# Optimization experiments

Hardware: AMD Instinct MI355X
Metric: run time of the kernel (lower is better)

The kernel has to match this reference:

```python
import jax, jax.numpy as jnp
import numpy as np

N_NODES = 10000
N_EDGES = 320000
IN_FEATS = 500
CONV_DIMS = [500, 256, 256]
FC_DIMS = [256, 128, 40]
BN_EPS = 1e-5


def setup_inputs() -> dict:
    key = jax.random.key(0)
    ks = jax.random.split(key, 16)
    inp = {
        "x": jax.random.normal(ks[0], (N_NODES, IN_FEATS), dtype=jnp.float32),
        "edge_index": jax.random.randint(ks[1], (2, N_EDGES), 0, N_NODES, dtype=jnp.int64),
    }
    # conv layer params: Linear W [in,out], b [out]; BatchNorm gamma/beta [out]
    ki = 2
    for li in range(len(CONV_DIMS) - 1):
        d_in, d_out = CONV_DIMS[li], CONV_DIMS[li + 1]
        s = 1.0 / np.sqrt(d_in)
        inp[f"conv_W{li}"] = jax.random.uniform(ks[ki], (d_in, d_out), jnp.float32, -s, s); ki += 1
        inp[f"conv_b{li}"] = jax.random.uniform(ks[ki], (d_out,), jnp.float32, -s, s); ki += 1
        inp[f"bn_g{li}"] = jnp.ones((d_out,), jnp.float32)
        inp[f"bn_b{li}"] = jnp.zeros((d_out,), jnp.float32)
    for li in range(len(FC_DIMS) - 1):
        d_in, d_out = FC_DIMS[li], FC_DIMS[li + 1]
        s = 1.0 / np.sqrt(d_in)
        inp[f"fc_W{li}"] = jax.random.uniform(ks[ki], (d_in, d_out), jnp.float32, -s, s); ki += 1
        inp[f"fc_b{li}"] = jax.random.uniform(ks[ki], (d_out,), jnp.float32, -s, s); ki += 1
    return inp


def _degree(edge_index, n, dtype):
    # Faithful to: A = eye(N); A[i,j] = 1 per edge (set semantics dedupes repeats).
    A = jnp.eye(n, dtype=dtype).at[edge_index[0], edge_index[1]].set(1.0)
    return A.sum(axis=1)  # deg_i = rowsum of A


def _batchnorm(h, g, b):
    # training-mode BatchNorm1d: batch stats, biased variance
    mean = h.mean(axis=0)
    var = h.var(axis=0)
    return (h - mean) * jax.lax.rsqrt(var + BN_EPS) * g + b


def reference(x, edge_index, conv_W0, conv_b0, bn_g0, bn_b0,
              conv_W1, conv_b1, bn_g1, bn_b1,
              fc_W0, fc_b0, fc_W1, fc_b1):
    n = x.shape[0]
    deg = _degree(edge_index, n, x.dtype)
    # D = sqrt(diag(deg)) is a diagonal matrix, so elementwise D*A*D = diag(deg);
    # mm(D*A*D, x) == deg[:, None] * x (exactly the original math).
    h = x
    for W, b, g, beta in ((conv_W0, conv_b0, bn_g0, bn_b0),
                          (conv_W1, conv_b1, bn_g1, bn_b1)):
        h = (deg[:, None] * h) @ W + b
        h = jax.nn.relu(h)
        h = _batchnorm(h, g, beta)
        # dropout: identity at inference
    for W, b in ((fc_W0, fc_b0), (fc_W1, fc_b1)):
        h = jax.nn.relu(h @ W + b)  # original appends ReLU after every fc, incl. last
    return h
```

## Files before the change

### kernel.cpp

```cpp
#include <hip/hip_runtime.h>

#define NN 10000
#define NE 320000
#define ROW_WORDS 320
#define MP 10112
#define BN_EPS 1e-5f

typedef __attribute__((ext_vector_type(8))) short short8;
typedef __attribute__((ext_vector_type(4))) float f32x4;
typedef unsigned short u16;

__device__ __forceinline__ void split1(float v, u16& h, u16& l) {
    unsigned int u = __float_as_uint(v);
    h = (u16)(u >> 16);
    float hf = __uint_as_float(u & 0xFFFF0000u);
    l = (u16)(__float_as_uint(v - hf) >> 16);
}

__device__ __forceinline__ void gll16(const void* g, void* l) {
    __builtin_amdgcn_global_load_lds(
        (const __attribute__((address_space(1))) unsigned int*)g,
        (__attribute__((address_space(3))) unsigned int*)l, 16, 0, 0);
}

__device__ void splitW_dev(const float* __restrict__ W, int K, int N, int Kp, int Np,
                           u16* __restrict__ Wt, int bx, int by, char* smem) {
    float (*tile)[65] = (float(*)[65])smem;
    int t = threadIdx.x;
    int bk = bx * 64, bn = by * 64;
    #pragma unroll
    for (int p = 0; p < 4; ++p) {
        int kk = (t >> 4) + p * 16;
        int nc = (t & 15) * 4;
        int k = bk + kk;
        float4 v = {0.f, 0.f, 0.f, 0.f};
        if (k < K && bn + nc + 3 < N)
            v = *(const float4*)&W[(size_t)k * N + bn + nc];
        tile[kk][nc] = v.x; tile[kk][nc + 1] = v.y;
        tile[kk][nc + 2] = v.z; tile[kk][nc + 3] = v.w;
    }
    __syncthreads();
    int nn = t >> 2;
    int kk0 = (t & 3) * 16;
    u16 hs[16], ls[16];
    #pragma unroll
    for (int j = 0; j < 16; ++j) split1(tile[kk0 + j][nn], hs[j], ls[j]);
    size_t ob = (size_t)(bn + nn) * Kp + bk + kk0;
    size_t lo = (size_t)Np * Kp;
    *(short8*)&Wt[ob] = *(short8*)hs;
    *(short8*)&Wt[ob + 8] = *(short8*)&hs[8];
    *(short8*)&Wt[lo + ob] = *(short8*)ls;
    *(short8*)&Wt[lo + ob + 8] = *(short8*)&ls[8];
}

__device__ void xsplit_dev(const float* __restrict__ x, u16* __restrict__ xs, int gblk) {
    int t = threadIdx.x;
    int r0 = gblk * 16 + (t >> 4);
    int l = t & 15;
    u16* xlo = xs + (size_t)MP * 512;
    #pragma unroll
    for (int j = 0; j < 8; ++j) {
        int k = (l + j * 16) * 4;
        float vals[4] = {0.f, 0.f, 0.f, 0.f};
        if (r0 < NN && k < 500) {
            float4 v = *(const float4*)&x[(size_t)r0 * 500 + k];
            vals[0] = v.x; vals[1] = v.y; vals[2] = v.z; vals[3] = v.w;
        }
        ushort4 hs, ls;
        split1(vals[0], hs.x, ls.x); split1(vals[1], hs.y, ls.y);
        split1(vals[2], hs.z, ls.z); split1(vals[3], hs.w, ls.w);
        *(ushort4*)&xs[(size_t)r0 * 512 + k] = hs;
        *(ushort4*)&xlo[(size_t)r0 * 512 + k] = ls;
    }
}

__global__ __launch_bounds__(256)
void scatter_prep(const int* __restrict__ ei, unsigned int* __restrict__ bitmap,
                  const float* __restrict__ x,
                  const float* __restrict__ W0, const float* __restrict__ fW1,
                  u16* __restrict__ xs, u16* __restrict__ W0t, u16* __restrict__ fW1t) {
    __shared__ char smem[16704];
    int b = blockIdx.x;
    if (b < 1290) {
        int e = b * 256 + threadIdx.x;
        if (e < NE + NN) {
            int i, j;
            if (e < NE) { i = ei[e]; j = ei[NE + e]; }
            else        { i = e - NE; j = i; }
            atomicOr(&bitmap[i * ROW_WORDS + (j >> 5)], 1u << (j & 31));
        }
    } else if (b < 1922) {
        xsplit_dev(x, xs, b - 1290);
    } else if (b < 1954) {
        int idx = b - 1922;
        splitW_dev(W0, 500, 256, 512, 256, W0t, idx & 7, idx >> 3, smem);
    } else {
        splitW_dev(fW1, 128, 40, 128, 64, fW1t, b - 1954, 0, smem);
    }
}

__global__ __launch_bounds__(256, 4)
void conv0_gemm(const u16* __restrict__ Ahi, const u16* __restrict__ Alo,
                const u16* __restrict__ Bhi, const u16* __restrict__ Blo,
                const unsigned int* __restrict__ bitmap, const float* __restrict__ bias,
                float* __restrict__ deg, float* __restrict__ stats,
                u16* __restrict__ Ohi, u16* __restrict__ Olo) {
    __shared__ char smem[32768];
    __shared__ float sdeg[64];
    const int Kp = 512, M = NN, No = 256;
    const int b = blockIdx.x;
    const int xcd = b & 7, g = b >> 3;
    const int bx = g & 3, by = (g >> 2) * 8 + xcd;
    if (by >= 158) return;
    const int t = threadIdx.x;
    const int lane = t & 63;
    const int w = t >> 6;
    const int q = lane >> 4;
    const int l16 = lane & 15;
    const int m7 = l16 & 7;
    const int row0 = by * 64;
    const int col0 = bx * 64;

    const u16* bases[4] = {Ahi, Alo, Bhi, Blo};
    const u16* srcs[8];
    unsigned dstoff[8];
    #pragma unroll
    for (int i = 0; i < 8; ++i) {
        int gi = w + i * 4;
        int reg = i >> 1;
        int j = gi & 7;
        int rb = (reg < 2) ? row0 : col0;
        int r = j * 8 + (lane >> 3);
        int c = (lane & 7) ^ (r & 7);
        srcs[i] = bases[reg] + (size_t)(rb + r) * Kp + c * 8;
        dstoff[i] = reg * 8192 + j * 1024;
    }

    f32x4 acc[4];
    #pragma unroll
    for (int s = 0; s < 4; ++s) acc[s] = (f32x4){0.f, 0.f, 0.f, 0.f};

    #pragma unroll
    for (int i = 0; i < 8; ++i) { gll16(srcs[i], smem + dstoff[i]); srcs[i] += 64; }

    {
        int rr = t >> 2, wl = t & 3;
        int grow = row0 + rr;
        int cnt = 0;
        if (grow < NN)
            for (int wd = wl; wd < ROW_WORDS; wd += 4)
                cnt += __popc(bitmap[(size_t)grow * ROW_WORDS + wd]);
        cnt += __shfl_down(cnt, 1, 4);
        cnt += __shfl_down(cnt, 2, 4);
        if (wl == 0) {
            sdeg[rr] = (float)cnt;
            if (bx == 0 && grow < NN) deg[grow] = (float)cnt;
        }
    }

    for (int k0 = 0; k0 < Kp; k0 += 64) {
        __syncthreads();
        short8 ah[2], al[2], bh[2][4], bl[2][4];
        #pragma unroll
        for (int kc = 0; kc < 2; ++kc) {
            int aoff = (w * 16 + l16) * 128 + (((kc * 4 + q) ^ m7) * 16);
            ah[kc] = *(const short8*)(smem + aoff);
            al[kc] = *(const short8*)(smem + 8192 + aoff);
            #pragma unroll
            for (int s = 0; s < 4; ++s) {
                int boff = (s * 16 + l16) * 128 + (((kc * 4 + q) ^ m7) * 16);
                bh[kc][s] = *(const short8*)(smem + 16384 + boff);
                bl[kc][s] = *(const short8*)(smem + 24576 + boff);
            }
        }
        __syncthreads();
        if (k0 + 64 < Kp) {
            #pragma unroll
            for (int i = 0; i < 8; ++i) { gll16(srcs[i], smem + dstoff[i]); srcs[i] += 64; }
        }
        #pragma unroll
        for (int kc = 0; kc < 2; ++kc)
            #pragma unroll
            for (int s = 0; s < 4; ++s) {
                acc[s] = __builtin_amdgcn_mfma_f32_16x16x32_bf16(al[kc], bh[kc][s], acc[s], 0, 0, 0);
                acc[s] = __builtin_amdgcn_mfma_f32_16x16x32_bf16(ah[kc], bl[kc][s], acc[s], 0, 0, 0);
                acc[s] = __builtin_amdgcn_mfma_f32_16x16x32_bf16(ah[kc], bh[kc][s], acc[s], 0, 0, 0);
            }
    }

    int growb = row0 + w * 16 + q * 4;
    float dgv[4];
    #pragma unroll
    for (int r = 0; r < 4; ++r) {
        int grow = growb + r;
        dgv[r] = (grow < M) ? sdeg[grow - row0] : 0.f;
    }
    #pragma unroll
    for (int s = 0; s < 4; ++s) {
        int gc = col0 + s * 16 + l16;
        float bia = bias[gc];
        float s_sum = 0.f, ss_sum = 0.f;
        #pragma unroll
        for (int r = 0; r < 4; ++r) {
            int grow = growb + r;
            bool real = grow < M;
            float v = fmaxf(fmaf(dgv[r], acc[s][r], bia), 0.f);
            if (!real) v = 0.f;
            s_sum += v; ss_sum += v * v;
            float vo = v * dgv[r];
            u16 h, l; split1(vo, h, l);
            Ohi[(size_t)grow * No + gc] = h;
            Olo[(size_t)grow * No + gc] = l;
        }
        s_sum  += __shfl_xor(s_sum, 16);  s_sum  += __shfl_xor(s_sum, 32);
        ss_sum += __shfl_xor(ss_sum, 16); ss_sum += __shfl_xor(ss_sum, 32);
        if (lane < 16) {
            atomicAdd(&stats[gc], s_sum);
            atomicAdd(&stats[256 + gc], ss_sum);
        }
    }
}

__global__ __launch_bounds__(256, 4)
void conv1_fold(const u16* __restrict__ Ahi, const u16* __restrict__ Alo,
                const float* __restrict__ W1, const float* __restrict__ stats0,
                const float* __restrict__ g0, const float* __restrict__ bb0,
                const float* __restrict__ b1, const float* __restrict__ deg,
                float* __restrict__ stats1, u16* __restrict__ Ohi, u16* __restrict__ Olo) {
    __shared__ char smem[32768];
    __shared__ float scl[256], sh[256], cred[256], cvec[64];
    const int Kp = 256, M = NN, No = 256;
    const int b = blockIdx.x;
    const int xcd = b & 7, g = b >> 3;
    const int bx = g & 3, by = (g >> 2) * 8 + xcd;
    if (by >= 158) return;
    const int t = threadIdx.x;
    const int lane = t & 63;
    const int w = t >> 6;
    const int q = lane >> 4;
    const int l16 = lane & 15;
    const int m7 = l16 & 7;
    const int row0 = by * 64;
    const int col0 = bx * 64;

    const u16* srcs[4];
    unsigned dstoff[4];
    #pragma unroll
    for (int i = 0; i < 4; ++i) {
        int gi = w + i * 4;
        int plane = gi >> 3, j = gi & 7;
        int r = j * 8 + (lane >> 3);
        int c = (lane & 7) ^ (r & 7);
        srcs[i] = (plane ? Alo : Ahi) + (size_t)(row0 + r) * Kp + c * 8;
        dstoff[i] = plane * 8192 + j * 1024;
    }
    #pragma unroll
    for (int i = 0; i < 4; ++i) { gll16(srcs[i], smem + dstoff[i]); srcs[i] += 64; }

    {
        float mean = stats0[t] * (1.f / NN);
        float var = stats0[256 + t] * (1.f / NN) - mean * mean;
        float s = g0[t] * rsqrtf(var + BN_EPS);
        scl[t] = s;
        sh[t] = bb0[t] - mean * s;
    }
    __syncthreads();
    {
        float s = 0.f;
        int n = col0 + (t & 63);
        #pragma unroll 8
        for (int k = (t >> 6); k < 256; k += 4)
            s += sh[k] * W1[(size_t)k * 256 + n];
        cred[t] = s;
        __syncthreads();
        if (t < 64) cvec[t] = cred[t] + cred[t + 64] + cred[t + 128] + cred[t + 192];
    }
    const int bn = t & 63;
    const int kb = (t >> 6) * 16;
    const int ch0 = (t >> 6) * 2;
    float vals[16];
    {
        const float* wp = W1 + (size_t)kb * 256 + col0 + bn;
        #pragma unroll
        for (int i = 0; i < 16; ++i) vals[i] = wp[(size_t)i * 256] * scl[kb + i];
    }

    f32x4 acc[4];
    #pragma unroll
    for (int s = 0; s < 4; ++s) acc[s] = (f32x4){0.f, 0.f, 0.f, 0.f};

    for (int k0 = 0; k0 < Kp; k0 += 64) {
        {
            u16 hs[16], ls[16];
            #pragma unroll
            for (int i = 0; i < 16; ++i) split1(vals[i], hs[i], ls[i]);
            unsigned o0 = bn * 128 + ((ch0 ^ (bn & 7)) * 16);
            unsigned o1 = bn * 128 + (((ch0 + 1) ^ (bn & 7)) * 16);
            *(short8*)(smem + 16384 + o0) = *(short8*)&hs[0];
            *(short8*)(smem + 16384 + o1) = *(short8*)&hs[8];
            *(short8*)(smem + 24576 + o0) = *(short8*)&ls[0];
            *(short8*)(smem + 24576 + o1) = *(short8*)&ls[8];
        }
        __syncthreads();
        short8 ah[2], al[2], bh[2][4], bl[2][4];
        #pragma unroll
        for (int kc = 0; kc < 2; ++kc) {
            int aoff = (w * 16 + l16) * 128 + (((kc * 4 + q) ^ m7) * 16);
            ah[kc] = *(const short8*)(smem + aoff);
            al[kc] = *(const short8*)(smem + 8192 + aoff);
            #pragma unroll
            for (int s = 0; s < 4; ++s) {
                int boff = (s * 16 + l16) * 128 + (((kc * 4 + q) ^ m7) * 16);
                bh[kc][s] = *(const short8*)(smem + 16384 + boff);
                bl[kc][s] = *(const short8*)(smem + 24576 + boff);
            }
        }
        __syncthreads();
        if (k0 + 64 < Kp) {
            #pragma unroll
            for (int i = 0; i < 4; ++i) { gll16(srcs[i], smem + dstoff[i]); srcs[i] += 64; }
            const float* wp = W1 + (size_t)(k0 + 64 + kb) * 256 + col0 + bn;
            #pragma unroll
            for (int i = 0; i < 16; ++i) vals[i] = wp[(size_t)i * 256] * scl[k0 + 64 + kb + i];
        }
        #pragma unroll
        for (int kc = 0; kc < 2; ++kc)
            #pragma unroll
            for (int s = 0; s < 4; ++s) {
                acc[s] = __builtin_amdgcn_mfma_f32_16x16x32_bf16(al[kc], bh[kc][s], acc[s], 0, 0, 0);
                acc[s] = __builtin_amdgcn_mfma_f32_16x16x32_bf16(ah[kc], bl[kc][s], acc[s], 0, 0, 0);
                acc[s] = __builtin_amdgcn_mfma_f32_16x16x32_bf16(ah[kc], bh[kc][s], acc[s], 0, 0, 0);
            }
    }

    int growb = row0 + w * 16 + q * 4;
    float dgv[4];
    #pragma unroll
    for (int r = 0; r < 4; ++r) dgv[r] = (growb + r < M) ? deg[growb + r] : 0.f;
    #pragma unroll
    for (int s = 0; s < 4; ++s) {
        int gc = col0 + s * 16 + l16;
        float bia = b1[gc];
        float cv = cvec[s * 16 + l16];
        float s_sum = 0.f, ss_sum = 0.f;
        #pragma unroll
        for (int r = 0; r < 4; ++r) {
            int grow = growb + r;
            bool real = grow < M;
            float v = fmaxf(fmaf(dgv[r], cv, acc[s][r] + bia), 0.f);
            if (!real) v = 0.f;
            s_sum += v; ss_sum += v * v;
            u16 h, l; split1(v, h, l);
            Ohi[(size_t)grow * No + gc] = h;
            Olo[(size_t)grow * No + gc] = l;
        }
        s_sum  += __shfl_xor(s_sum, 16);  s_sum  += __shfl_xor(s_sum, 32);
        ss_sum += __shfl_xor(ss_sum, 16); ss_sum += __shfl_xor(ss_sum, 32);
        if (lane < 16) {
            atomicAdd(&stats1[gc], s_sum);
            atomicAdd(&stats1[256 + gc], ss_sum);
        }
    }
}

__global__ __launch_bounds__(256, 4)
void fc0_fold(const u16* __restrict__ Ahi, const u16* __restrict__ Alo,
              const float* __restrict__ fW0, const float* __restrict__ stats1,
              const float* __restrict__ g1, const float* __restrict__ bb1,
              const float* __restrict__ fb0,
              u16* __restrict__ Ohi, u16* __restrict__ Olo) {
    __shared__ char smem[32768];
    __shared__ float scl[256], sh[256], cred[256], biasf[64];
    const int Kp = 256, M = NN, No = 128;
    const int b = blockIdx.x;
    const int xcd = b & 7, g = b >> 3;
    const int bx = g & 1, by = (g >> 1) * 8 + xcd;
    if (by >= 158) return;
    const int t = threadIdx.x;
    const int lane = t & 63;
    const int w = t >> 6;
    const int q = lane >> 4;
    const int l16 = lane & 15;
    const int m7 = l16 & 7;
    const int row0 = by * 64;
    const int col0 = bx * 64;

    const u16* srcs[4];
    unsigned dstoff[4];
    #pragma unroll
    for (int i = 0; i < 4; ++i) {
        int gi = w + i * 4;
        int plane = gi >> 3, j = gi & 7;
        int r = j * 8 + (lane >> 3);
        int c = (lane & 7) ^ (r & 7);
        srcs[i] = (plane ? Alo : Ahi) + (size_t)(row0 + r) * Kp + c * 8;
        dstoff[i] = plane * 8192 + j * 1024;
    }
    #pragma unroll
    for (int i = 0; i < 4; ++i) { gll16(srcs[i], smem + dstoff[i]); srcs[i] += 64; }

    {
        float mean = stats1[t] * (1.f / NN);
        float var = stats1[256 + t] * (1.f / NN) - mean * mean;
        float s = g1[t] * rsqrtf(var + BN_EPS);
        scl[t] = s;
        sh[t] = bb1[t] - mean * s;
    }
    __syncthreads();
    {
        float s = 0.f;
        int n = col0 + (t & 63);
        #pragma unroll 8
        for (int k = (t >> 6); k < 256; k += 4)
            s += sh[k] * fW0[(size_t)k * 128 + n];
        cred[t] = s;
        __syncthreads();
        if (t < 64)
            biasf[t] = fb0[col0 + t] + cred[t] + cred[t + 64] + cred[t + 128] + cred[t + 192];
    }
    const int bn = t & 63;
    const int kb = (t >> 6) * 16;
    const int ch0 = (t >> 6) * 2;
    float vals[16];
    {
        const float* wp = fW0 + (size_t)kb * 128 + col0 + bn;
        #pragma unroll
        for (int i = 0; i < 16; ++i) vals[i] = wp[(size_t)i * 128] * scl[kb + i];
    }

    f32x4 acc[4];
    #pragma unroll
    for (int s = 0; s < 4; ++s) acc[s] = (f32x4){0.f, 0.f, 0.f, 0.f};

    for (int k0 = 0; k0 < Kp; k0 += 64) {
        {
            u16 hs[16], ls[16];
            #pragma unroll
            for (int i = 0; i < 16; ++i) split1(vals[i], hs[i], ls[i]);
            unsigned o0 = bn * 128 + ((ch0 ^ (bn & 7)) * 16);
            unsigned o1 = bn * 128 + (((ch0 + 1) ^ (bn & 7)) * 16);
            *(short8*)(smem + 16384 + o0) = *(short8*)&hs[0];
            *(short8*)(smem + 16384 + o1) = *(short8*)&hs[8];
            *(short8*)(smem + 24576 + o0) = *(short8*)&ls[0];
            *(short8*)(smem + 24576 + o1) = *(short8*)&ls[8];
        }
        __syncthreads();
        short8 ah[2], al[2], bh[2][4], bl[2][4];
        #pragma unroll
        for (int kc = 0; kc < 2; ++kc) {
            int aoff = (w * 16 + l16) * 128 + (((kc * 4 + q) ^ m7) * 16);
            ah[kc] = *(const short8*)(smem + aoff);
            al[kc] = *(const short8*)(smem + 8192 + aoff);
            #pragma unroll
            for (int s = 0; s < 4; ++s) {
                int boff = (s * 16 + l16) * 128 + (((kc * 4 + q) ^ m7) * 16);
                bh[kc][s] = *(const short8*)(smem + 16384 + boff);
                bl[kc][s] = *(const short8*)(smem + 24576 + boff);
            }
        }
        __syncthreads();
        if (k0 + 64 < Kp) {
            #pragma unroll
            for (int i = 0; i < 4; ++i) { gll16(srcs[i], smem + dstoff[i]); srcs[i] += 64; }
            const float* wp = fW0 + (size_t)(k0 + 64 + kb) * 128 + col0 + bn;
            #pragma unroll
            for (int i = 0; i < 16; ++i) vals[i] = wp[(size_t)i * 128] * scl[k0 + 64 + kb + i];
        }
        #pragma unroll
        for (int kc = 0; kc < 2; ++kc)
            #pragma unroll
            for (int s = 0; s < 4; ++s) {
                acc[s] = __builtin_amdgcn_mfma_f32_16x16x32_bf16(al[kc], bh[kc][s], acc[s], 0, 0, 0);
                acc[s] = __builtin_amdgcn_mfma_f32_16x16x32_bf16(ah[kc], bl[kc][s], acc[s], 0, 0, 0);
                acc[s] = __builtin_amdgcn_mfma_f32_16x16x32_bf16(ah[kc], bh[kc][s], acc[s], 0, 0, 0);
            }
    }

    int growb = row0 + w * 16 + q * 4;
    #pragma unroll
    for (int s = 0; s < 4; ++s) {
        int gc = col0 + s * 16 + l16;
        float bia = biasf[s * 16 + l16];
        #pragma unroll
        for (int r = 0; r < 4; ++r) {
            int grow = growb + r;
            float v = fmaxf(acc[s][r] + bia, 0.f);
            if (grow >= M) v = 0.f;
            u16 h, l; split1(v, h, l);
            Ohi[(size_t)grow * No + gc] = h;
            Olo[(size_t)grow * No + gc] = l;
        }
    }
}

__global__ __launch_bounds__(256, 3)
void fc1_gemm(const u16* __restrict__ Ahi, const u16* __restrict__ Alo,
              const u16* __restrict__ Bhi, const u16* __restrict__ Blo,
              const float* __restrict__ bias, float* __restrict__ out) {
    __shared__ char smem[32768];
    const int Kp = 128, M = NN, N = 40, No = 40;
    const int t = threadIdx.x;
    const int lane = t & 63;
    const int w = t >> 6;
    const int q = lane >> 4;
    const int l16 = lane & 15;
    const int m7 = l16 & 7;
    const int row0 = blockIdx.x * 64;
    const int col0 = 0;

    const u16* bases[4] = {Ahi, Alo, Bhi, Blo};
    const u16* srcs[8];
    unsigned dstoff[8];
    #pragma unroll
    for (int i = 0; i < 8; ++i) {
        int gi = w + i * 4;
        int reg = i >> 1;
        int j = gi & 7;
        int rb = (reg < 2) ? row0 : col0;
        int r = j * 8 + (lane >> 3);
        int c = (lane & 7) ^ (r & 7);
        srcs[i] = bases[reg] + (size_t)(rb + r) * Kp + c * 8;
        dstoff[i] = reg * 8192 + j * 1024;
    }

    f32x4 acc[4];
    #pragma unroll
    for (int s = 0; s < 4; ++s) acc[s] = (f32x4){0.f, 0.f, 0.f, 0.f};

    #pragma unroll
    for (int i = 0; i < 8; ++i) { gll16(srcs[i], smem + dstoff[i]); srcs[i] += 64; }

    for (int k0 = 0; k0 < Kp; k0 += 64) {
        __syncthreads();
        short8 ah[2], al[2], bh[2][4], bl[2][4];
        #pragma unroll
        for (int kc = 0; kc < 2; ++kc) {
            int aoff = (w * 16 + l16) * 128 + (((kc * 4 + q) ^ m7) * 16);
            ah[kc] = *(const short8*)(smem + aoff);
            al[kc] = *(const short8*)(smem + 8192 + aoff);
            #pragma unroll
            for (int s = 0; s < 4; ++s) {
                int boff = (s * 16 + l16) * 128 + (((kc * 4 + q) ^ m7) * 16);
                bh[kc][s] = *(const short8*)(smem + 16384 + boff);
                bl[kc][s] = *(const short8*)(smem + 24576 + boff);
            }
        }
        __syncthreads();
        if (k0 + 64 < Kp) {
            #pragma unroll
            for (int i = 0; i < 8; ++i) { gll16(srcs[i], smem + dstoff[i]); srcs[i] += 64; }
        }
        #pragma unroll
        for (int kc = 0; kc < 2; ++kc)
            #pragma unroll
            for (int s = 0; s < 4; ++s) {
                acc[s] = __builtin_amdgcn_mfma_f32_16x16x32_bf16(al[kc], bh[kc][s], acc[s], 0, 0, 0);
                acc[s] = __builtin_amdgcn_mfma_f32_16x16x32_bf16(ah[kc], bl[kc][s], acc[s], 0, 0, 0);
                acc[s] = __builtin_amdgcn_mfma_f32_16x16x32_bf16(ah[kc], bh[kc][s], acc[s], 0, 0, 0);
            }
    }

    int growb = row0 + w * 16 + q * 4;
    #pragma unroll
    for (int s = 0; s < 4; ++s) {
        int gc = col0 + s * 16 + l16;
        if (gc >= N) continue;
        float bia = bias[gc];
        #pragma unroll
        for (int r = 0; r < 4; ++r) {
            int grow = growb + r;
            if (grow < M)
                out[(size_t)grow * No + gc] = fmaxf(acc[s][r] + bia, 0.f);
        }
    }
}


extern "C" void kernel_launch(void* const* d_in, const int* in_sizes, int n_in,
                              void* d_out, int out_size, void* d_ws, size_t ws_size,
                              hipStream_t stream) {
    const float* x   = (const float*)d_in[0];
    const int*   ei  = (const int*)d_in[1];
    const float* W0  = (const float*)d_in[2];
    const float* b0  = (const float*)d_in[3];
    const float* g0  = (const float*)d_in[4];
    const float* bb0 = (const float*)d_in[5];
    const float* W1  = (const float*)d_in[6];
    const float* b1  = (const float*)d_in[7];
    const float* g1  = (const float*)d_in[8];
    const float* bb1 = (const float*)d_in[9];
    const float* fW0 = (const float*)d_in[10];
    const float* fb0 = (const float*)d_in[11];
    const float* fW1 = (const float*)d_in[12];
    const float* fb1 = (const float*)d_in[13];
    float* out = (float*)d_out;

    char* ws = (char*)d_ws;
    auto carve = [&](size_t bytes) { char* q = ws; ws += (bytes + 255) & ~(size_t)255; return q; };

    const size_t BITMAP_BYTES = (size_t)NN * ROW_WORDS * 4;
    char* region0 = carve(BITMAP_BYTES + 4096);
    unsigned int* bitmap = (unsigned int*)region0;
    float* stats = (float*)(region0 + BITMAP_BYTES);

    float* deg  = (float*)carve(MP * 4);
    u16* xs     = (u16*)carve((size_t)2 * MP * 512 * 2);
    u16* W0t    = (u16*)carve((size_t)2 * 256 * 512 * 2);
    u16* fW1t   = (u16*)carve((size_t)2 * 64 * 128 * 2);
    u16* H1     = (u16*)carve((size_t)2 * MP * 256 * 2);
    u16* H2     = (u16*)carve((size_t)2 * MP * 256 * 2);
    u16* H3     = (u16*)carve((size_t)2 * MP * 128 * 2);

    dim3 blk(256);

    hipMemsetAsync(region0, 0, BITMAP_BYTES + 4096, stream);
    scatter_prep<<<1956, blk, 0, stream>>>(ei, bitmap, x, W0, fW1, xs, W0t, fW1t);
    conv0_gemm<<<640, blk, 0, stream>>>(
        xs, xs + (size_t)MP * 512, W0t, W0t + 256 * 512,
        bitmap, b0, deg, stats, H1, H1 + (size_t)MP * 256);
    conv1_fold<<<640, blk, 0, stream>>>(
        H1, H1 + (size_t)MP * 256, W1, stats, g0, bb0, b1, deg,
        stats + 512, H2, H2 + (size_t)MP * 256);
    fc0_fold<<<320, blk, 0, stream>>>(
        H2, H2 + (size_t)MP * 256, fW0, stats + 512, g1, bb1, fb0,
        H3, H3 + (size_t)MP * 128);
    fc1_gemm<<<158, blk, 0, stream>>>(
        H3, H3 + (size_t)MP * 128, fW1t, fW1t + 64 * 128, fb1, out);
}
```

Before: 188.0 us.

## Fuse fc0 and fc1 GEMMs into one kernel keeping hidden tile in LDS

Merges the fc0 fold GEMM and the fc1 GEMM into a single kernel. Each block computes both 64-column halves of the 128-wide hidden layer for its 64 rows, keeps the split bf16 hi/lo results in registers and then LDS, and multiplies them by fW1 directly. This removes one kernel launch and the H3 write and read through global memory. In exchange the grid shrinks from 320 to 157 blocks, each block rereads its A tile twice, and occupancy drops with 48KB of LDS and launch bounds of 2.

```diff
diff --git a/kernel.cpp b/kernel.cpp
--- a/kernel.cpp
+++ b/kernel.cpp
@@ -363,19 +363,17 @@
     }
 }
 
-__global__ __launch_bounds__(256, 4)
-void fc0_fold(const u16* __restrict__ Ahi, const u16* __restrict__ Alo,
+__global__ __launch_bounds__(256, 2)
+void fc_fused(const u16* __restrict__ Ahi, const u16* __restrict__ Alo,
               const float* __restrict__ fW0, const float* __restrict__ stats1,
               const float* __restrict__ g1, const float* __restrict__ bb1,
               const float* __restrict__ fb0,
-              u16* __restrict__ Ohi, u16* __restrict__ Olo) {
-    __shared__ char smem[32768];
-    __shared__ float scl[256], sh[256], cred[256], biasf[64];
-    const int Kp = 256, M = NN, No = 128;
-    const int b = blockIdx.x;
-    const int xcd = b & 7, g = b >> 3;
-    const int bx = g & 1, by = (g >> 1) * 8 + xcd;
-    if (by >= 158) return;
+              const u16* __restrict__ Whi, const u16* __restrict__ Wlo,
+              const float* __restrict__ fb1, float* __restrict__ out) {
+    __shared__ char smem[49152];
+    __shared__ float scl[256], sh[256], cred[256], biasf[128];
+    const int M = NN;
+    const int by = blockIdx.x;
     const int t = threadIdx.x;
     const int lane = t & 63;
     const int w = t >> 6;
@@ -383,21 +381,20 @@
     const int l16 = lane & 15;
     const int m7 = l16 & 7;
     const int row0 = by * 64;
-    const int col0 = bx * 64;
-
-    const u16* srcs[4];
-    unsigned dstoff[4];
+
+    const u16* asrc[4];
+    unsigned adst[4];
     #pragma unroll
     for (int i = 0; i < 4; ++i) {
         int gi = w + i * 4;
         int plane = gi >> 3, j = gi & 7;
         int r = j * 8 + (lane >> 3);
         int c = (lane & 7) ^ (r & 7);
-        srcs[i] = (plane ? Alo : Ahi) + (size_t)(row0 + r) * Kp + c * 8;
-        dstoff[i] = plane * 8192 + j * 1024;
-    }
-    #pragma unroll
-    for (int i = 0; i < 4; ++i) { gll16(srcs[i], smem + dstoff[i]); srcs[i] += 64; }
+        asrc[i] = (plane ? Alo : Ahi) + (size_t)(row0 + r) * 256 + c * 8;
+        adst[i] = plane * 8192 + j * 1024;
+    }
+    #pragma unroll
+    for (int i = 0; i < 4; ++i) gll16(asrc[i], smem + adst[i]);
 
     {
         float mean = stats1[t] * (1.f / NN);
@@ -408,63 +405,158 @@
     }
     __syncthreads();
     {
+        int col = t & 127, half = t >> 7;
         float s = 0.f;
-        int n = col0 + (t & 63);
         #pragma unroll 8
-        for (int k = (t >> 6); k < 256; k += 4)
-            s += sh[k] * fW0[(size_t)k * 128 + n];
+        for (int k = half * 128; k < half * 128 + 128; ++k)
+            s += sh[k] * fW0[(size_t)k * 128 + col];
         cred[t] = s;
-        __syncthreads();
-        if (t < 64)
-            biasf[t] = fb0[col0 + t] + cred[t] + cred[t + 64] + cred[t + 128] + cred[t + 192];
-    }
+    }
+    __syncthreads();
+    if (t < 128) biasf[t] = fb0[t] + cred[t] + cred[128 + t];
+
     const int bn = t & 63;
     const int kb = (t >> 6) * 16;
     const int ch0 = (t >> 6) * 2;
-    float vals[16];
-    {
-        const float* wp = fW0 + (size_t)kb * 128 + col0 + bn;
-        #pragma unroll
-        for (int i = 0; i < 16; ++i) vals[i] = wp[(size_t)i * 128] * scl[kb + i];
-    }
-
+
+    unsigned h3p[2][16];
     f32x4 acc[4];
+
+    #pragma unroll
+    for (int sub = 0; sub < 2; ++sub) {
+        if (sub) {
+            #pragma unroll
+            for (int i = 0; i < 4; ++i) { asrc[i] -= 192; gll16(asrc[i], smem + adst[i]); }
+        }
+        float vals[16];
+        {
+            const float* wp = fW0 + (size_t)kb * 128 + sub * 64 + bn;
+            #pragma unroll
+            for (int i = 0; i < 16; ++i) vals[i] = wp[(size_t)i * 128] * scl[kb + i];
+        }
+        #pragma unroll
+        for (int s = 0; s < 4; ++s) acc[s] = (f32x4){0.f, 0.f, 0.f, 0.f};
+
+        for (int k0 = 0; k0 < 256; k0 += 64) {
+            {
+                u16 hs[16], ls[16];
+                #pragma unroll
+                for (int i = 0; i < 16; ++i) split1(vals[i], hs[i], ls[i]);
+                unsigned o0 = bn * 128 + ((ch0 ^ (bn & 7)) * 16);
+                unsigned o1 = bn * 128 + (((ch0 + 1) ^ (bn & 7)) * 16);
+                *(short8*)(smem + 16384 + o0) = *(short8*)&hs[0];
+                *(short8*)(smem + 16384 + o1) = *(short8*)&hs[8];
+                *(short8*)(smem + 24576 + o0) = *(short8*)&ls[0];
+                *(short8*)(smem + 24576 + o1) = *(short8*)&ls[8];
+            }
+            __syncthreads();
+            short8 ah[2], al[2], bh[2][4], bl[2][4];
+            #pragma unroll
+            for (int kc = 0; kc < 2; ++kc) {
+                int aoff = (w * 16 + l16) * 128 + (((kc * 4 + q) ^ m7) * 16);
+                ah[kc] = *(const short8*)(smem + aoff);
+                al[kc] = *(const short8*)(smem + 8192 + aoff);
+                #pragma unroll
+                for (int s = 0; s < 4; ++s) {
+                    int boff = (s * 16 + l16) * 128 + (((kc * 4 + q) ^ m7) * 16);
+                    bh[kc][s] = *(const short8*)(smem + 16384 + boff);
+                    bl[kc][s] = *(const short8*)(smem + 24576 + boff);
+                }
+            }
+            __syncthreads();
+            if (k0 + 64 < 256) {
+                #pragma unroll
+                for (int i = 0; i < 4; ++i) { asrc[i] += 64; gll16(asrc[i], smem + adst[i]); }
+                const float* wp = fW0 + (size_t)(k0 + 64 + kb) * 128 + sub * 64 + bn;
+                #pragma unroll
+                for (int i = 0; i < 16; ++i) vals[i] = wp[(size_t)i * 128] * scl[k0 + 64 + kb + i];
+            }
+            #pragma unroll
+            for (int kc = 0; kc < 2; ++kc)
+                #pragma unroll
+                for (int s = 0; s < 4; ++s) {
+                    acc[s] = __builtin_amdgcn_mfma_f32_16x16x32_bf16(al[kc], bh[kc][s], acc[s], 0, 0, 0);
+                    acc[s] = __builtin_amdgcn_mfma_f32_16x16x32_bf16(ah[kc], bl[kc][s], acc[s], 0, 0, 0);
+                    acc[s] = __builtin_amdgcn_mfma_f32_16x16x32_bf16(ah[kc], bh[kc][s], acc[s], 0, 0, 0);
+                }
+        }
+
+        {
+            int growb = row0 + w * 16 + q * 4;
+            #pragma unroll
+            for (int s = 0; s < 4; ++s) {
+                float bia = biasf[sub * 64 + s * 16 + l16];
+                #pragma unroll
+                for (int r = 0; r < 4; ++r) {
+                    float v = fmaxf(acc[s][r] + bia, 0.f);
+                    if (growb + r >= M) v = 0.f;
+                    u16 h, l; split1(v, h, l);
+                    h3p[sub][s * 4 + r] = ((unsigned)h << 16) | l;
+                }
+            }
+        }
+    }
+
+    #pragma unroll
+    for (int i = 0; i < 4; ++i) {
+        int gi = w + i * 4;
+        int plane = gi >> 3, j = gi & 7;
+        int r = j * 8 + (lane >> 3);
+        int c = (lane & 7) ^ (r & 7);
+        const u16* s = (plane ? Wlo : Whi) + (size_t)r * 128 + c * 8;
+        gll16(s, smem + 32768 + plane * 8192 + j * 1024);
+    }
+
+    {
+        int rl0 = w * 16 + q * 4;
+        #pragma unroll
+        for (int sub = 0; sub < 2; ++sub)
+            #pragma unroll
+            for (int s = 0; s < 4; ++s)
+                #pragma unroll
+                for (int r = 0; r < 4; ++r) {
+                    int rl = rl0 + r;
+                    int kk = s * 16 + l16;
+                    int j = kk >> 3;
+                    unsigned off = (unsigned)sub * 8192 + rl * 128 +
+                                   ((j ^ (rl & 7)) * 16) + (kk & 7) * 2;
+                    unsigned pv = h3p[sub][s * 4 + r];
+                    *(u16*)(smem + off) = (u16)(pv >> 16);
+                    *(u16*)(smem + 16384 + off) = (u16)pv;
+                }
+    }
+
     #pragma unroll
     for (int s = 0; s < 4; ++s) acc[s] = (f32x4){0.f, 0.f, 0.f, 0.f};
 
-    for (int k0 = 0; k0 < Kp; k0 += 64) {
-        {
-            u16 hs[16], ls[16];
-            #pragma unroll
-            for (int i = 0; i < 16; ++i) split1(vals[i], hs[i], ls[i]);
-            unsigned o0 = bn * 128 + ((ch0 ^ (bn & 7)) * 16);
-            unsigned o1 = bn * 128 + (((ch0 + 1) ^ (bn & 7)) * 16);
-            *(short8*)(smem + 16384 + o0) = *(short8*)&hs[0];
-            *(short8*)(smem + 16384 + o1) = *(short8*)&hs[8];
-            *(short8*)(smem + 24576 + o0) = *(short8*)&ls[0];
-            *(short8*)(smem + 24576 + o1) = *(short8*)&ls[8];
+    __syncthreads();
+
+    #pragma unroll
+    for (int st = 0; st < 2; ++st) {
+        short8 ah[2], al[2], bh[2][4], bl[2][4];
+        #pragma unroll
+        for (int kc = 0; kc < 2; ++kc) {
+            int aoff = st * 8192 + (w * 16 + l16) * 128 + (((kc * 4 + q) ^ m7) * 16);
+            ah[kc] = *(const short8*)(smem + aoff);
+            al[kc] = *(const short8*)(smem + 16384 + aoff);
+            #pragma unroll
+            for (int s = 0; s < 4; ++s) {
+                int boff = 32768 + (s * 16 + l16) * 128 + (((kc * 4 + q) ^ m7) * 16);
+                bh[kc][s] = *(const short8*)(smem + boff);
+                bl[kc][s] = *(const short8*)(smem + 8192 + boff);
+            }
         }
         __syncthreads();
-        short8 ah[2], al[2], bh[2][4], bl[2][4];
-        #pragma unroll
-        for (int kc = 0; kc < 2; ++kc) {
-            int aoff = (w * 16 + l16) * 128 + (((kc * 4 + q) ^ m7) * 16);
-            ah[kc] = *(const short8*)(smem + aoff);
-            al[kc] = *(const short8*)(smem + 8192 + aoff);
-            #pragma unroll
-            for (int s = 0; s < 4; ++s) {
-                int boff = (s * 16 + l16) * 128 + (((kc * 4 + q) ^ m7) * 16);
-                bh[kc][s] = *(const short8*)(smem + 16384 + boff);
-                bl[kc][s] = *(const short8*)(smem + 24576 + boff);
-            }
-        }
-        __syncthreads();
-        if (k0 + 64 < Kp) {
-            #pragma unroll
-            for (int i = 0; i < 4; ++i) { gll16(srcs[i], smem + dstoff[i]); srcs[i] += 64; }
-            const float* wp = fW0 + (size_t)(k0 + 64 + kb) * 128 + col0 + bn;
-            #pragma unroll
-            for (int i = 0; i < 16; ++i) vals[i] = wp[(size_t)i * 128] * scl[k0 + 64 + kb + i];
+        if (st == 0) {
+            #pragma unroll
+            for (int i = 0; i < 4; ++i) {
+                int gi = w + i * 4;
+                int plane = gi >> 3, j = gi & 7;
+                int r = j * 8 + (lane >> 3);
+                int c = (lane & 7) ^ (r & 7);
+                const u16* s = (plane ? Wlo : Whi) + (size_t)r * 128 + 64 + c * 8;
+                gll16(s, smem + 32768 + plane * 8192 + j * 1024);
+            }
         }
         #pragma unroll
         for (int kc = 0; kc < 2; ++kc)
@@ -474,103 +566,22 @@
                 acc[s] = __builtin_amdgcn_mfma_f32_16x16x32_bf16(ah[kc], bl[kc][s], acc[s], 0, 0, 0);
                 acc[s] = __builtin_amdgcn_mfma_f32_16x16x32_bf16(ah[kc], bh[kc][s], acc[s], 0, 0, 0);
             }
-    }
-
-    int growb = row0 + w * 16 + q * 4;
-    #pragma unroll
-    for (int s = 0; s < 4; ++s) {
-        int gc = col0 + s * 16 + l16;
-        float bia = biasf[s * 16 + l16];
-        #pragma unroll
-        for (int r = 0; r < 4; ++r) {
-            int grow = growb + r;
-            float v = fmaxf(acc[s][r] + bia, 0.f);
-            if (grow >= M) v = 0.f;
-            u16 h, l; split1(v, h, l);
-            Ohi[(size_t)grow * No + gc] = h;
-            Olo[(size_t)grow * No + gc] = l;
-        }
-    }
-}
-
-__global__ __launch_bounds__(256, 3)
-void fc1_gemm(const u16* __restrict__ Ahi, const u16* __restrict__ Alo,
-              const u16* __restrict__ Bhi, const u16* __restrict__ Blo,
-              const float* __restrict__ bias, float* __restrict__ out) {
-    __shared__ char smem[32768];
-    const int Kp = 128, M = NN, N = 40, No = 40;
-    const int t = threadIdx.x;
-    const int lane = t & 63;
-    const int w = t >> 6;
-    const int q = lane >> 4;
-    const int l16 = lane & 15;
-    const int m7 = l16 & 7;
-    const int row0 = blockIdx.x * 64;
-    const int col0 = 0;
-
-    const u16* bases[4] = {Ahi, Alo, Bhi, Blo};
-    const u16* srcs[8];
-    unsigned dstoff[8];
-    #pragma unroll
-    for (int i = 0; i < 8; ++i) {
-        int gi = w + i * 4;
-        int reg = i >> 1;
-        int j = gi & 7;
-        int rb = (reg < 2) ? row0 : col0;
-        int r = j * 8 + (lane >> 3);
-        int c = (lane & 7) ^ (r & 7);
-        srcs[i] = bases[reg] + (size_t)(rb + r) * Kp + c * 8;
-        dstoff[i] = reg * 8192 + j * 1024;
-    }
-
-    f32x4 acc[4];
-    #pragma unroll
-    for (int s = 0; s < 4; ++s) acc[s] = (f32x4){0.f, 0.f, 0.f, 0.f};
-
-    #pragma unroll
-    for (int i = 0; i < 8; ++i) { gll16(srcs[i], smem + dstoff[i]); srcs[i] += 64; }
-
-    for (int k0 = 0; k0 < Kp; k0 += 64) {
-        __syncthreads();
-        short8 ah[2], al[2], bh[2][4], bl[2][4];
-        #pragma unroll
-        for (int kc = 0; kc < 2; ++kc) {
-            int aoff = (w * 16 + l16) * 128 + (((kc * 4 + q) ^ m7) * 16);
-            ah[kc] = *(const short8*)(smem + aoff);
-            al[kc] = *(const short8*)(smem + 8192 + aoff);
-            #pragma unroll
-            for (int s = 0; s < 4; ++s) {
-                int boff = (s * 16 + l16) * 128 + (((kc * 4 + q) ^ m7) * 16);
-                bh[kc][s] = *(const short8*)(smem + 16384 + boff);
-                bl[kc][s] = *(const short8*)(smem + 24576 + boff);
-            }
-        }
-        __syncthreads();
-        if (k0 + 64 < Kp) {
-            #pragma unroll
-            for (int i = 0; i < 8; ++i) { gll16(srcs[i], smem + dstoff[i]); srcs[i] += 64; }
-        }
-        #pragma unroll
-        for (int kc = 0; kc < 2; ++kc)
-            #pragma unroll
-            for (int s = 0; s < 4; ++s) {
-                acc[s] = __builtin_amdgcn_mfma_f32_16x16x32_bf16(al[kc], bh[kc][s], acc[s], 0, 0, 0);
-                acc[s] = __builtin_amdgcn_mfma_f32_16x16x32_bf16(ah[kc], bl[kc][s], acc[s], 0, 0, 0);
-                acc[s] = __builtin_amdgcn_mfma_f32_16x16x32_bf16(ah[kc], bh[kc][s], acc[s], 0, 0, 0);
-            }
-    }
-
-    int growb = row0 + w * 16 + q * 4;
-    #pragma unroll
-    for (int s = 0; s < 4; ++s) {
-        int gc = col0 + s * 16 + l16;
-        if (gc >= N) continue;
-        float bia = bias[gc];
-        #pragma unroll
-        for (int r = 0; r < 4; ++r) {
-            int grow = growb + r;
-            if (grow < M)
-                out[(size_t)grow * No + gc] = fmaxf(acc[s][r] + bia, 0.f);
+        if (st == 0) __syncthreads();
+    }
+
+    {
+        int growb = row0 + w * 16 + q * 4;
+        #pragma unroll
+        for (int s = 0; s < 4; ++s) {
+            int gc = s * 16 + l16;
+            if (gc >= 40) continue;
+            float bia = fb1[gc];
+            #pragma unroll
+            for (int r = 0; r < 4; ++r) {
+                int grow = growb + r;
+                if (grow < M)
+                    out[(size_t)grow * 40 + gc] = fmaxf(acc[s][r] + bia, 0.f);
+            }
         }
     }
 }
@@ -609,7 +620,6 @@
     u16* fW1t   = (u16*)carve((size_t)2 * 64 * 128 * 2);
     u16* H1     = (u16*)carve((size_t)2 * MP * 256 * 2);
     u16* H2     = (u16*)carve((size_t)2 * MP * 256 * 2);
-    u16* H3     = (u16*)carve((size_t)2 * MP * 128 * 2);
 
     dim3 blk(256);
 
@@ -621,9 +631,7 @@
     conv1_fold<<<640, blk, 0, stream>>>(
         H1, H1 + (size_t)MP * 256, W1, stats, g0, bb0, b1, deg,
         stats + 512, H2, H2 + (size_t)MP * 256);
-    fc0_fold<<<320, blk, 0, stream>>>(
+    fc_fused<<<157, blk, 0, stream>>>(
         H2, H2 + (size_t)MP * 256, fW0, stats + 512, g1, bb1, fb0,
-        H3, H3 + (size_t)MP * 128);
-    fc1_gemm<<<158, blk, 0, stream>>>(
-        H3, H3 + (size_t)MP * 128, fW1t, fW1t + 64 * 128, fb1, out);
-}
+        fW1t, fW1t + 64 * 128, fb1, out);
+}
```

After: 190.8 us. Within noise of the previous version (+1.5%).

## Replace global dense adjacency bitmap with bucketed edges and LDS-local dedup bitmaps

Applied to the files above, without the earlier changes.

The global 12.8MB adjacency bitmap, with its memset and scattered global atomics, is replaced by a two-pass scheme. Edges are binned into buckets by row range and column half, then a new kernel builds a per-bucket bitmap in shared memory to deduplicate edges and popcounts rows into degree. conv0_gemm now just reads the precomputed degree. This removes the large memset and the global atomic and bitmap traffic, at the cost of an extra kernel launch and a fixed bucket capacity that silently drops edges if a bucket overflows.

```diff
diff --git a/kernel.cpp b/kernel.cpp
--- a/kernel.cpp
+++ b/kernel.cpp
@@ -2,9 +2,16 @@
 
 #define NN 10000
 #define NE 320000
-#define ROW_WORDS 320
 #define MP 10112
 #define BN_EPS 1e-5f
+
+#define NRANGE 64
+#define BROWS 160
+#define NBUCK 128
+#define HBITS 5120
+#define HWORDS 160
+#define BCAP  4096
+#define EPB   5000
 
 typedef __attribute__((ext_vector_type(8))) short short8;
 typedef __attribute__((ext_vector_type(4))) float f32x4;
@@ -75,35 +82,108 @@
 }
 
 __global__ __launch_bounds__(256)
-void scatter_prep(const int* __restrict__ ei, unsigned int* __restrict__ bitmap,
+void scatter_prep(const int* __restrict__ ei,
+                  unsigned* __restrict__ bucketArr, unsigned* __restrict__ gcount,
                   const float* __restrict__ x,
                   const float* __restrict__ W0, const float* __restrict__ fW1,
                   u16* __restrict__ xs, u16* __restrict__ W0t, u16* __restrict__ fW1t) {
     __shared__ char smem[16704];
+    __shared__ unsigned cnt[NBUCK], basep[NBUCK];
     int b = blockIdx.x;
-    if (b < 1290) {
-        int e = b * 256 + threadIdx.x;
-        if (e < NE + NN) {
-            int i, j;
-            if (e < NE) { i = ei[e]; j = ei[NE + e]; }
-            else        { i = e - NE; j = i; }
-            atomicOr(&bitmap[i * ROW_WORDS + (j >> 5)], 1u << (j & 31));
-        }
-    } else if (b < 1922) {
-        xsplit_dev(x, xs, b - 1290);
-    } else if (b < 1954) {
-        int idx = b - 1922;
+    int t = threadIdx.x;
+    if (b < 64) {
+        if (t < NBUCK) cnt[t] = 0;
+        __syncthreads();
+        int base = b * EPB;
+        unsigned myb[20], myk[20];
+        #pragma unroll
+        for (int k = 0; k < 20; ++k) {
+            int el = t + k * 256;
+            myb[k] = 0xFFFFFFFFu;
+            if (el < EPB) {
+                int e = base + el;
+                unsigned i = (unsigned)ei[e], j = (unsigned)ei[NE + e];
+                unsigned bk = (i / BROWS) * 2 + (j >= HBITS ? 1u : 0u);
+                myb[k] = bk;
+                myk[k] = (i << 14) | j;
+                atomicAdd(&cnt[bk], 1u);
+            }
+        }
+        __syncthreads();
+        if (t < NBUCK) { basep[t] = atomicAdd(&gcount[t * 16], cnt[t]); cnt[t] = 0; }
+        __syncthreads();
+        #pragma unroll
+        for (int k = 0; k < 20; ++k) {
+            if (myb[k] != 0xFFFFFFFFu) {
+                unsigned bk = myb[k];
+                unsigned pos = basep[bk] + atomicAdd(&cnt[bk], 1u);
+                if (pos < BCAP) bucketArr[(size_t)bk * BCAP + pos] = myk[k];
+            }
+        }
+    } else if (b < 696) {
+        xsplit_dev(x, xs, b - 64);
+    } else if (b < 728) {
+        int idx = b - 696;
         splitW_dev(W0, 500, 256, 512, 256, W0t, idx & 7, idx >> 3, smem);
     } else {
-        splitW_dev(fW1, 128, 40, 128, 64, fW1t, b - 1954, 0, smem);
+        splitW_dev(fW1, 128, 40, 128, 64, fW1t, b - 728, 0, smem);
+    }
+}
+
+__global__ __launch_bounds__(256)
+void bucket_degree(const unsigned* __restrict__ bucketArr,
+                   const unsigned* __restrict__ gcount,
+                   float* __restrict__ deg) {
+    __shared__ unsigned lbm[BROWS * HWORDS];
+    int b = blockIdx.x, t = threadIdx.x;
+    int rr = b >> 1, h = b & 1;
+    int row0 = rr * BROWS;
+    {
+        uint4* z = (uint4*)lbm;
+        #pragma unroll
+        for (int i = 0; i < 25; ++i) z[t + i * 256] = (uint4){0u, 0u, 0u, 0u};
+    }
+    __syncthreads();
+    for (int r = t; r < BROWS; r += 256) {
+        int i = row0 + r;
+        if (i < NN && ((i >= HBITS) == (h == 1))) {
+            int jj = i - h * HBITS;
+            atomicOr(&lbm[r * HWORDS + (jj >> 5)], 1u << (jj & 31));
+        }
+    }
+    unsigned n = gcount[b * 16];
+    const unsigned* keys = bucketArr + (size_t)b * BCAP;
+    for (unsigned k = t; k < n; k += 256) {
+        unsigned key = keys[k];
+        unsigned i = key >> 14, j = key & 0x3FFFu;
+        unsigned r = i - row0;
+        unsigned jj = j - h * HBITS;
+        atomicOr(&lbm[r * HWORDS + (jj >> 5)], 1u << (jj & 31));
+    }
+    __syncthreads();
+    #pragma unroll
+    for (int pass = 0; pass < 3; ++pass) {
+        int r = pass * 64 + (t >> 2), wl = t & 3;
+        if (r >= BROWS) break;
+        int i = row0 + r;
+        int c = 0;
+        const uint4* rp = (const uint4*)&lbm[r * HWORDS + wl * 40];
+        #pragma unroll
+        for (int m = 0; m < 10; ++m) {
+            uint4 v = rp[m];
+            c += __popc(v.x) + __popc(v.y) + __popc(v.z) + __popc(v.w);
+        }
+        c += __shfl_down(c, 1, 4);
+        c += __shfl_down(c, 2, 4);
+        if (wl == 0 && i < NN) atomicAdd(&deg[i], (float)c);
     }
 }
 
 __global__ __launch_bounds__(256, 4)
 void conv0_gemm(const u16* __restrict__ Ahi, const u16* __restrict__ Alo,
                 const u16* __restrict__ Bhi, const u16* __restrict__ Blo,
-                const unsigned int* __restrict__ bitmap, const float* __restrict__ bias,
-                float* __restrict__ deg, float* __restrict__ stats,
+                const float* __restrict__ deg, const float* __restrict__ bias,
+                float* __restrict__ stats,
                 u16* __restrict__ Ohi, u16* __restrict__ Olo) {
     __shared__ char smem[32768];
     __shared__ float sdeg[64];
@@ -143,20 +223,7 @@
     #pragma unroll
     for (int i = 0; i < 8; ++i) { gll16(srcs[i], smem + dstoff[i]); srcs[i] += 64; }
 
-    {
-        int rr = t >> 2, wl = t & 3;
-        int grow = row0 + rr;
-        int cnt = 0;
-        if (grow < NN)
-            for (int wd = wl; wd < ROW_WORDS; wd += 4)
-                cnt += __popc(bitmap[(size_t)grow * ROW_WORDS + wd]);
-        cnt += __shfl_down(cnt, 1, 4);
-        cnt += __shfl_down(cnt, 2, 4);
-        if (wl == 0) {
-            sdeg[rr] = (float)cnt;
-            if (bx == 0 && grow < NN) deg[grow] = (float)cnt;
-        }
-    }
+    if (t < 64) sdeg[t] = deg[row0 + t];
 
     for (int k0 = 0; k0 < Kp; k0 += 64) {
         __syncthreads();
@@ -598,12 +665,13 @@
     char* ws = (char*)d_ws;
     auto carve = [&](size_t bytes) { char* q = ws; ws += (bytes + 255) & ~(size_t)255; return q; };
 
-    const size_t BITMAP_BYTES = (size_t)NN * ROW_WORDS * 4;
-    char* region0 = carve(BITMAP_BYTES + 4096);
-    unsigned int* bitmap = (unsigned int*)region0;
-    float* stats = (float*)(region0 + BITMAP_BYTES);
-
-    float* deg  = (float*)carve(MP * 4);
+    const size_t ZERO_BYTES = 4096 + 8192 + (size_t)MP * 4;
+    char* region0 = carve(ZERO_BYTES);
+    float* stats = (float*)region0;
+    unsigned* gcount = (unsigned*)(region0 + 4096);
+    float* deg   = (float*)(region0 + 4096 + 8192);
+
+    unsigned* bucketArr = (unsigned*)carve((size_t)NBUCK * BCAP * 4);
     u16* xs     = (u16*)carve((size_t)2 * MP * 512 * 2);
     u16* W0t    = (u16*)carve((size_t)2 * 256 * 512 * 2);
     u16* fW1t   = (u16*)carve((size_t)2 * 64 * 128 * 2);
@@ -613,11 +681,12 @@
 
     dim3 blk(256);
 
-    hipMemsetAsync(region0, 0, BITMAP_BYTES + 4096, stream);
-    scatter_prep<<<1956, blk, 0, stream>>>(ei, bitmap, x, W0, fW1, xs, W0t, fW1t);
+    hipMemsetAsync(region0, 0, ZERO_BYTES, stream);
+    scatter_prep<<<730, blk, 0, stream>>>(ei, bucketArr, gcount, x, W0, fW1, xs, W0t, fW1t);
+    bucket_degree<<<NBUCK, blk, 0, stream>>>(bucketArr, gcount, deg);
     conv0_gemm<<<640, blk, 0, stream>>>(
         xs, xs + (size_t)MP * 512, W0t, W0t + 256 * 512,
-        bitmap, b0, deg, stats, H1, H1 + (size_t)MP * 256);
+        deg, b0, stats, H1, H1 + (size_t)MP * 256);
     conv1_fold<<<640, blk, 0, stream>>>(
         H1, H1 + (size_t)MP * 256, W1, stats, g0, bb0, b1, deg,
         stats + 512, H2, H2 + (size_t)MP * 256);
```

Measured after the change: 179.9 us. -4.3%, faster.
